# Kernel optimization log

Hardware: AMD Instinct MI355X
Metric: run time of the kernel (lower is better)

Reference implementation:

```python
import jax, jax.numpy as jnp
import numpy as np

B, L, D = 4, 2048, 32

def setup_inputs() -> dict:
    key = jax.random.key(0)
    k1, k2 = jax.random.split(key)
    dz = jax.random.normal(k1, (B, L, D), dtype=jnp.float32)
    Gamma = jax.random.normal(k2, (B, L, D, D, D), dtype=jnp.float32)
    return {"dz": dz, "Gamma": Gamma}

def reference(dz, Gamma):
    # a_geo^k = -Gamma^k_ij dz^i dz^j, per (b, l)
    # Single fused contraction reading Gamma once: [B,L,D,D,D] x [B,L,D] x [B,L,D] -> [B,L,D]
    return -jnp.einsum('blkij,bli,blj->blk', Gamma, dz, dz)
```

## Files before the change

### kernel.cpp

```cpp
#include <hip/hip_runtime.h>


#define D 32

__global__ __launch_bounds__(256) void geodesic_accel_kernel(
    const float* __restrict__ dz,
    const float* __restrict__ Gamma,
    float* __restrict__ out)
{
    const int bl = blockIdx.x;
    const float* __restrict__ G = Gamma + (size_t)bl * (D * D * D);
    const float* __restrict__ z = dz + (size_t)bl * D;
    float* __restrict__ o = out + (size_t)bl * D;

    const int tid  = threadIdx.x;
    const int wave = tid >> 6;
    const int lane = tid & 63;

    const int j0 = (lane & 7) * 4;
    const float4 zj = *reinterpret_cast<const float4*>(z + j0);

    const int ibase = lane >> 3;
    float4 w4[4];
#pragma unroll
    for (int m = 0; m < 4; ++m) {
        const float zi = z[m * 8 + ibase];
        w4[m] = make_float4(zi * zj.x, zi * zj.y, zi * zj.z, zi * zj.w);
    }

#pragma unroll
    for (int s = 0; s < 8; ++s) {
        const int k = wave * 8 + s;
        const float4* __restrict__ Gk =
            reinterpret_cast<const float4*>(G + k * (D * D));
        float acc = 0.f;
#pragma unroll
        for (int m = 0; m < 4; ++m) {
            const float4 g = Gk[m * 64 + lane];
            acc += g.x * w4[m].x + g.y * w4[m].y + g.z * w4[m].z + g.w * w4[m].w;
        }
#pragma unroll
        for (int off = 32; off > 0; off >>= 1) {
            acc += __shfl_xor(acc, off);
        }
        if (lane == 0) {
            o[k] = -acc;
        }
    }
}

extern "C" void kernel_launch(void* const* d_in, const int* in_sizes, int n_in,
                              void* d_out, int out_size, void* d_ws, size_t ws_size,
                              hipStream_t stream)
{
    const float* dz    = (const float*)d_in[0];
    const float* Gamma = (const float*)d_in[1];
    float* out         = (float*)d_out;

    const int n_bl = in_sizes[0] / D;
    geodesic_accel_kernel<<<n_bl, 256, 0, stream>>>(dz, Gamma, out);
}
```

Measured before the change: 189.3 us.

## Interleave k-slices with nontemporal loads and a transposed butterfly reduction

Swaps the loop order so each wave keeps eight accumulators and issues all 32 vector loads of Gamma across its eight k-slices together, giving more memory-level parallelism. The loads are marked nontemporal because Gamma is streamed once. The eight separate 6-step shuffle reductions become a transposed butterfly that packs partial sums across lanes, cutting the shuffle count. Lanes 0-7 then write the eight outputs. The costs are more live registers and a kernel whose time stays bound by HBM bandwidth, so the room for gain is small.

After: 167.8 us. 1.13x faster.

```diff
diff --git a/kernel.cpp b/kernel.cpp
--- a/kernel.cpp
+++ b/kernel.cpp
@@ -2,6 +2,14 @@
 
 
 #define D 32
+
+typedef float f32x4 __attribute__((ext_vector_type(4)));
+
+__device__ __forceinline__ float red_step(float a, float b, int off, int lane) {
+    float t = (lane & off) ? a : b;
+    t = __shfl_xor(t, off);
+    return (lane & off) ? (b + t) : (a + t);
+}
 
 __global__ __launch_bounds__(256) void geodesic_accel_kernel(
     const float* __restrict__ dz,
@@ -18,34 +26,47 @@
     const int lane = tid & 63;
 
     const int j0 = (lane & 7) * 4;
-    const float4 zj = *reinterpret_cast<const float4*>(z + j0);
+    const f32x4 zj = *reinterpret_cast<const f32x4*>(z + j0);
 
     const int ibase = lane >> 3;
-    float4 w4[4];
+    f32x4 w4[4];
 #pragma unroll
     for (int m = 0; m < 4; ++m) {
         const float zi = z[m * 8 + ibase];
-        w4[m] = make_float4(zi * zj.x, zi * zj.y, zi * zj.z, zi * zj.w);
+        w4[m] = zi * zj;
     }
 
+    const f32x4* __restrict__ Gw =
+        reinterpret_cast<const f32x4*>(G + (wave * 8) * (D * D));
+
+    float acc[8] = {0.f, 0.f, 0.f, 0.f, 0.f, 0.f, 0.f, 0.f};
+
 #pragma unroll
-    for (int s = 0; s < 8; ++s) {
-        const int k = wave * 8 + s;
-        const float4* __restrict__ Gk =
-            reinterpret_cast<const float4*>(G + k * (D * D));
-        float acc = 0.f;
+    for (int m = 0; m < 4; ++m) {
+        const f32x4 w = w4[m];
 #pragma unroll
-        for (int m = 0; m < 4; ++m) {
-            const float4 g = Gk[m * 64 + lane];
-            acc += g.x * w4[m].x + g.y * w4[m].y + g.z * w4[m].z + g.w * w4[m].w;
+        for (int s = 0; s < 8; ++s) {
+            const f32x4 g = __builtin_nontemporal_load(Gw + s * 256 + m * 64 + lane);
+            acc[s] = fmaf(g.x, w.x,
+                     fmaf(g.y, w.y,
+                     fmaf(g.z, w.z,
+                     fmaf(g.w, w.w, acc[s]))));
         }
-#pragma unroll
-        for (int off = 32; off > 0; off >>= 1) {
-            acc += __shfl_xor(acc, off);
-        }
-        if (lane == 0) {
-            o[k] = -acc;
-        }
+    }
+
+    float r0 = red_step(acc[0], acc[1], 1, lane);
+    float r1 = red_step(acc[2], acc[3], 1, lane);
+    float r2 = red_step(acc[4], acc[5], 1, lane);
+    float r3 = red_step(acc[6], acc[7], 1, lane);
+    float s0 = red_step(r0, r1, 2, lane);
+    float s1 = red_step(r2, r3, 2, lane);
+    float t0 = red_step(s0, s1, 4, lane);
+    t0 += __shfl_xor(t0, 8);
+    t0 += __shfl_xor(t0, 16);
+    t0 += __shfl_xor(t0, 32);
+
+    if (lane < 8) {
+        o[wave * 8 + lane] = -t0;
     }
 }
 
```
